# Kernel optimization log

Hardware: AMD Instinct MI355X
Metric: run time of the kernel (lower is better)

## Reference

```python
import jax, jax.numpy as jnp
import numpy as np

E = 16      # num_experts
H = 1024    # hidden_size
O = 1       # output_size
B = 4096    # batch
K = 2       # top-k (hard-coded in module)


def setup_inputs() -> dict:
    key = jax.random.key(0)
    ks = jax.random.split(key, 7)
    s_h = 1.0 / np.sqrt(H)
    inp = {
        "embeddings": jax.random.normal(ks[0], (B, H), dtype=jnp.float32),
        "router_w": jax.random.uniform(ks[1], (H, E), jnp.float32, -s_h, s_h),
        "router_b": jax.random.uniform(ks[2], (E,), jnp.float32, -s_h, s_h),
        "w1": jax.random.uniform(ks[3], (E, H, H), jnp.float32, -s_h, s_h),
        "b1": jax.random.uniform(ks[4], (E, H), jnp.float32, -s_h, s_h),
        "w2": jax.random.uniform(ks[5], (E, H, O), jnp.float32, -s_h, s_h),
        "b2": jax.random.uniform(ks[6], (E, O), jnp.float32, -s_h, s_h),
    }
    return inp


def reference(embeddings, router_w, router_b, w1, b1, w2, b2):
    # Router: top-2 experts per token, softmax over the 2 selected logits.
    logits = embeddings @ router_w + router_b                 # [B, E]
    top_vals, top_idx = jax.lax.top_k(logits, K)              # [B, K]
    top_w = jax.nn.softmax(top_vals, axis=-1)                 # [B, K]

    # Per-expert combine weight: w_e[b] = sum_k top_w[b,k] * (top_idx[b,k]==e)
    onehot = (top_idx[:, :, None] == jnp.arange(E)[None, None, :])  # [B, K, E]
    comb = jnp.einsum('bk,bke->eb', top_w, onehot.astype(top_w.dtype))  # [E, B]

    # Dense per-expert 2-layer MLP (small fixed E); masked-weighted combine
    # reproduces the gather/scatter-add exactly.
    h = jax.nn.relu(jnp.einsum('bh,ehd->ebd', embeddings, w1) + b1[:, None, :])  # [E, B, H]
    out = jnp.einsum('ebd,edo->ebo', h, w2) + b2[:, None, :]                      # [E, B, O]
    prediction = jnp.einsum('eb,ebo->bo', comb, out)                              # [B, O]
    return prediction
```

## Files before the change

kernel.cpp:

```cpp
#include <hip/hip_runtime.h>
#include <hip/hip_bf16.h>
#include <stdint.h>

#define E_EXP 16
#define H_DIM 1024
#define B_TOK 4096
#define BK 64
#define GBM 128
#define GBN 64
#define NSLOT 32
#define KS 16
#define KC 64
#define RTM 128
#define RSTRIDE (KC + 4)

typedef short bf16x8 __attribute__((ext_vector_type(8)));
typedef float f32x4 __attribute__((ext_vector_type(4)));

__device__ __forceinline__ unsigned short f2bf(float x) {
  union { float f; unsigned u; } v; v.f = x;
  unsigned r = v.u + 0x7FFFu + ((v.u >> 16) & 1u);
  return (unsigned short)(r >> 16);
}

__device__ __forceinline__ void gload_lds16(const void* g, void* l) {
  __builtin_amdgcn_global_load_lds(
      (const __attribute__((address_space(1))) void*)g,
      (__attribute__((address_space(3))) void*)l, 16, 0, 0);
}

__global__ __launch_bounds__(256) void k_prep(
    const float* __restrict__ emb, const float* __restrict__ rw,
    const float* __restrict__ w1, unsigned short* __restrict__ emb_bf,
    float* __restrict__ part, unsigned short* __restrict__ w1t)
{
  __shared__ __align__(16) char smem[RTM * RSTRIDE * 4 + KC * E_EXP * 4];
  const int tid = threadIdx.x;

  if (blockIdx.x < 512) {
    float* embL = (float*)smem;
    float* rwL  = (float*)(smem + RTM * RSTRIDE * 4);
    const int t0 = (blockIdx.x & 31) * RTM;
    const int ks = blockIdx.x >> 5;

#pragma unroll
    for (int it = 0; it < 8; ++it) {
      const int i = tid + 256 * it;
      const int row = i >> 4;
      const int c4 = i & 15;
      const size_t goff = (size_t)(t0 + row) * H_DIM + ks * KC + c4 * 4;
      const f32x4 v = *(const f32x4*)(emb + goff);
      ushort4 o;
      o.x = f2bf(v[0]); o.y = f2bf(v[1]); o.z = f2bf(v[2]); o.w = f2bf(v[3]);
      *(ushort4*)(emb_bf + goff) = o;
      *(f32x4*)(embL + row * RSTRIDE + c4 * 4) = v;
    }
    {
      const f32x4 v = *(const f32x4*)(rw + (size_t)ks * (KC * E_EXP) + tid * 4);
      *(f32x4*)(rwL + tid * 4) = v;
    }
    __syncthreads();

    const int w = tid >> 6, lane = tid & 63;
    const int tg = lane & 15, eg = lane >> 4;
    const int ta = w * 32 + tg, tb = ta + 16;

    f32x4 accA = {0.f, 0.f, 0.f, 0.f};
    f32x4 accB = {0.f, 0.f, 0.f, 0.f};
#pragma unroll
    for (int k4 = 0; k4 < KC / 4; ++k4) {
      const f32x4 e0 = *(const f32x4*)(embL + ta * RSTRIDE + k4 * 4);
      const f32x4 e1 = *(const f32x4*)(embL + tb * RSTRIDE + k4 * 4);
#pragma unroll
      for (int h = 0; h < 4; ++h) {
        const f32x4 r = *(const f32x4*)(rwL + (k4 * 4 + h) * E_EXP + eg * 4);
        accA += e0[h] * r;
        accB += e1[h] * r;
      }
    }
    *(f32x4*)(part + ((size_t)ks * B_TOK + t0 + ta) * E_EXP + eg * 4) = accA;
    *(f32x4*)(part + ((size_t)ks * B_TOK + t0 + tb) * E_EXP + eg * 4) = accB;
  } else {
    typedef unsigned short TileT[65];
    TileT* tile = (TileT*)smem;
    const int wb = blockIdx.x - 512;
    const int e  = wb >> 8;
    const int ht = (wb >> 4) & 15;
    const int dt = wb & 15;
    const float* src = w1 + ((size_t)e * H_DIM + ht * 64) * H_DIM + dt * 64;
    const int tr = tid >> 4;
    const int tc = tid & 15;
#pragma unroll
    for (int i = 0; i < 4; ++i) {
      const int r = tr + i * 16;
      const float4 v = *(const float4*)(src + (size_t)r * H_DIM + tc * 4);
      tile[r][tc * 4 + 0] = f2bf(v.x);
      tile[r][tc * 4 + 1] = f2bf(v.y);
      tile[r][tc * 4 + 2] = f2bf(v.z);
      tile[r][tc * 4 + 3] = f2bf(v.w);
    }
    __syncthreads();
    unsigned short* dst = w1t + ((size_t)e * H_DIM + dt * 64) * H_DIM + ht * 64;
    const int wr = tid >> 3;
    const int wc = tid & 7;
#pragma unroll
    for (int i = 0; i < 2; ++i) {
      const int r = wr + i * 32;
      ushort4 t0, t1;
      t0.x = tile[wc * 8 + 0][r]; t0.y = tile[wc * 8 + 1][r];
      t0.z = tile[wc * 8 + 2][r]; t0.w = tile[wc * 8 + 3][r];
      t1.x = tile[wc * 8 + 4][r]; t1.y = tile[wc * 8 + 5][r];
      t1.z = tile[wc * 8 + 6][r]; t1.w = tile[wc * 8 + 7][r];
      *(ushort4*)(dst + (size_t)r * H_DIM + wc * 8) = t0;
      *(ushort4*)(dst + (size_t)r * H_DIM + wc * 8 + 4) = t1;
    }
  }
}

__global__ __launch_bounds__(256) void k_router_select(
    const float* __restrict__ part, const float* __restrict__ rb,
    int* __restrict__ counts, int* __restrict__ lists,
    int4* __restrict__ meta, float2* __restrict__ wts)
{
  __shared__ int lcnt[E_EXP];
  __shared__ int base[E_EXP];
  const int tid = threadIdx.x;
  const int t = blockIdx.x * 256 + tid;
  if (tid < E_EXP) lcnt[tid] = 0;

  float lg[16];
#pragma unroll
  for (int q = 0; q < 4; ++q) {
    const f32x4 b = *(const f32x4*)(rb + q * 4);
    lg[q * 4 + 0] = b[0]; lg[q * 4 + 1] = b[1];
    lg[q * 4 + 2] = b[2]; lg[q * 4 + 3] = b[3];
  }
#pragma unroll
  for (int s = 0; s < KS; ++s) {
#pragma unroll
    for (int q = 0; q < 4; ++q) {
      const f32x4 v = *(const f32x4*)(part + ((size_t)s * B_TOK + t) * E_EXP + q * 4);
      lg[q * 4 + 0] += v[0]; lg[q * 4 + 1] += v[1];
      lg[q * 4 + 2] += v[2]; lg[q * 4 + 3] += v[3];
    }
  }

  float best = -1e30f; int b0 = 0;
#pragma unroll
  for (int e = 0; e < 16; ++e)
    if (lg[e] > best) { best = lg[e]; b0 = e; }
  float best2 = -1e30f; int b1i = 0;
#pragma unroll
  for (int e = 0; e < 16; ++e)
    if (e != b0 && lg[e] > best2) { best2 = lg[e]; b1i = e; }

  __syncthreads();
  const int l0 = atomicAdd(&lcnt[b0], 1);
  const int l1 = atomicAdd(&lcnt[b1i], 1);
  __syncthreads();
  if (tid < E_EXP) base[tid] = atomicAdd(&counts[tid], lcnt[tid]);
  __syncthreads();

  const int p0 = base[b0] + l0;
  const int p1 = base[b1i] + l1;
  lists[b0 * B_TOK + p0] = t;
  lists[b1i * B_TOK + p1] = t;
  meta[t] = make_int4(b0, b1i, p0, p1);
  const float e1v = expf(best2 - best);
  const float w0 = 1.f / (1.f + e1v);
  wts[t] = make_float2(w0, e1v * w0);
}

__global__ __launch_bounds__(256, 4) void k_moe_gemm(
    const unsigned short* __restrict__ emb_bf,
    const unsigned short* __restrict__ w1t,
    const float* __restrict__ b1, const float* __restrict__ w2,
    const int* __restrict__ counts, const int* __restrict__ lists,
    float* __restrict__ outbuf)
{
  const int bid = blockIdx.x;
  const int xcd = bid & 7;
  const int j = bid >> 3;
  const int e  = xcd + 8 * (j >> 7);
  const int r  = j & 127;
  const int nb = r >> 3;
  const int mbg = r & 7;
  const int cnt = counts[e];

  __shared__ unsigned short lA[GBM * BK];
  __shared__ unsigned short lB[GBN * BK];
  __shared__ int toks[GBM];

  const int tid = threadIdx.x;
  const int w = tid >> 6, lane = tid & 63;
  const int scb = ((lane & 7) * 16) ^ ((lane >> 3) << 4);
  const int wm = w >> 1, wn = w & 1;
  const int lr = lane & 15, lg = lane >> 4;

  const unsigned short* w1tb = w1t + ((size_t)e * H_DIM + nb * GBN) * H_DIM;
  const float* b1e = b1 + (size_t)e * H_DIM + nb * GBN;
  const float* w2e = w2 + (size_t)e * H_DIM + nb * GBN;

  const unsigned short* bSrc[2];
#pragma unroll
  for (int i = 0; i < 2; ++i) {
    const int n = (w * 2 + i) * 8 + (lane >> 3);
    bSrc[i] = w1tb + (size_t)n * H_DIM + (scb >> 1);
  }

  for (int mb = mbg; mb * GBM < cnt; mb += 8) {
    if (tid < GBM) {
      const int p = mb * GBM + tid;
      toks[tid] = lists[e * B_TOK + (p < cnt ? p : 0)];
    }
    __syncthreads();

    const unsigned short* aSrc[4];
#pragma unroll
    for (int i = 0; i < 4; ++i) {
      const int row = (w * 4 + i) * 8 + (lane >> 3);
      aSrc[i] = emb_bf + (size_t)toks[row] * H_DIM + (scb >> 1);
    }

    f32x4 acc[4][2];
#pragma unroll
    for (int m = 0; m < 4; ++m)
#pragma unroll
      for (int n = 0; n < 2; ++n) acc[m][n] = (f32x4){0.f, 0.f, 0.f, 0.f};

    for (int k0 = 0; k0 < H_DIM; k0 += BK) {
#pragma unroll
      for (int i = 0; i < 4; ++i)
        gload_lds16(aSrc[i] + k0, (char*)lA + (w * 4 + i) * 1024);
#pragma unroll
      for (int i = 0; i < 2; ++i)
        gload_lds16(bSrc[i] + k0, (char*)lB + (w * 2 + i) * 1024);
      __syncthreads();

#pragma unroll
      for (int kk = 0; kk < 2; ++kk) {
        const int kb = kk * 64 + lg * 16;
        bf16x8 af[4], bfr[2];
#pragma unroll
        for (int m = 0; m < 4; ++m) {
          const int row = wm * 64 + m * 16 + lr;
          af[m] = *(const bf16x8*)((const char*)lA + row * 128 + (kb ^ ((row & 7) << 4)));
        }
#pragma unroll
        for (int n = 0; n < 2; ++n) {
          const int row = wn * 32 + n * 16 + lr;
          bfr[n] = *(const bf16x8*)((const char*)lB + row * 128 + (kb ^ ((row & 7) << 4)));
        }
        __builtin_amdgcn_s_setprio(1);
#pragma unroll
        for (int m = 0; m < 4; ++m)
#pragma unroll
          for (int n = 0; n < 2; ++n)
            acc[m][n] = __builtin_amdgcn_mfma_f32_16x16x32_bf16(af[m], bfr[n], acc[m][n], 0, 0, 0);
        __builtin_amdgcn_s_setprio(0);
      }
      __syncthreads();
    }

    float rs[4][4];
#pragma unroll
    for (int m = 0; m < 4; ++m)
#pragma unroll
      for (int r4 = 0; r4 < 4; ++r4) rs[m][r4] = 0.f;

#pragma unroll
    for (int n = 0; n < 2; ++n) {
      const int d = wn * 32 + n * 16 + lr;
      const float bb = b1e[d];
      const float ww = w2e[d];
#pragma unroll
      for (int m = 0; m < 4; ++m)
#pragma unroll
        for (int r4 = 0; r4 < 4; ++r4) {
          float v = acc[m][n][r4] + bb;
          v = fmaxf(v, 0.f);
          rs[m][r4] = fmaf(v, ww, rs[m][r4]);
        }
    }
#pragma unroll
    for (int mask = 8; mask >= 1; mask >>= 1) {
#pragma unroll
      for (int m = 0; m < 4; ++m)
#pragma unroll
        for (int r4 = 0; r4 < 4; ++r4) rs[m][r4] += __shfl_xor(rs[m][r4], mask, 64);
    }

    if (lr == 0) {
      const int slot = nb * 2 + wn;
      float* ob = outbuf + ((size_t)slot * E_EXP + e) * B_TOK + mb * GBM;
#pragma unroll
      for (int m = 0; m < 4; ++m)
#pragma unroll
        for (int r4 = 0; r4 < 4; ++r4)
          ob[wm * 64 + m * 16 + lg * 4 + r4] = rs[m][r4];
    }
    __syncthreads();
  }
}

__global__ __launch_bounds__(256) void k_combine(
    const int4* __restrict__ meta, const float2* __restrict__ wts,
    const float* __restrict__ outbuf, const float* __restrict__ b2,
    float* __restrict__ out)
{
  const int t = blockIdx.x * 256 + threadIdx.x;
  if (t >= B_TOK) return;
  const int4 m = meta[t];
  const float2 w = wts[t];
  float o0 = b2[m.x], o1 = b2[m.y];
#pragma unroll
  for (int s = 0; s < NSLOT; ++s) {
    o0 += outbuf[((size_t)s * E_EXP + m.x) * B_TOK + m.z];
    o1 += outbuf[((size_t)s * E_EXP + m.y) * B_TOK + m.w];
  }
  out[t] = w.x * o0 + w.y * o1;
}

extern "C" void kernel_launch(void* const* d_in, const int* in_sizes, int n_in,
                              void* d_out, int out_size, void* d_ws, size_t ws_size,
                              hipStream_t stream)
{
  const float* emb = (const float*)d_in[0];
  const float* rw  = (const float*)d_in[1];
  const float* rb  = (const float*)d_in[2];
  const float* w1  = (const float*)d_in[3];
  const float* b1  = (const float*)d_in[4];
  const float* w2  = (const float*)d_in[5];
  const float* b2  = (const float*)d_in[6];
  float* out = (float*)d_out;

  char* ws = (char*)d_ws;
  size_t cur = 0;
  auto alloc = [&](size_t bytes) -> void* {
    void* p = ws + cur;
    cur += (bytes + 255) & ~(size_t)255;
    return p;
  };
  int*            counts = (int*)alloc(64);
  int4*           meta   = (int4*)alloc((size_t)B_TOK * 16);
  float2*         wts    = (float2*)alloc((size_t)B_TOK * 8);
  int*            lists  = (int*)alloc((size_t)E_EXP * B_TOK * 4);
  float*          outbuf = (float*)alloc((size_t)NSLOT * E_EXP * B_TOK * 4);
  float*          part   = (float*)alloc((size_t)KS * B_TOK * E_EXP * 4);
  unsigned short* emb_bf = (unsigned short*)alloc((size_t)B_TOK * H_DIM * 2);
  unsigned short* w1t    = (unsigned short*)alloc((size_t)E_EXP * H_DIM * H_DIM * 2);

  hipMemsetAsync(counts, 0, 64, stream);
  k_prep<<<dim3(512 + 4096), 256, 0, stream>>>(emb, rw, w1, emb_bf, part, w1t);
  k_router_select<<<B_TOK / 256, 256, 0, stream>>>(part, rb, counts, lists, meta, wts);
  k_moe_gemm<<<dim3(2048), 256, 0, stream>>>(emb_bf, w1t, b1, w2, counts, lists, outbuf);
  k_combine<<<B_TOK / 256, 256, 0, stream>>>(meta, wts, outbuf, b2, out);
}
```

Before: 85.64 us.

## Switch MoE GEMM to single-wave 64x64 tiles and fold counts reset into prep

The MoE GEMM goes from 256-thread blocks with 128x64 tiles to single-wavefront 64-thread blocks with 64x64 tiles, launching twice as many blocks. Because each block is one wave, the __syncthreads barriers become explicit waitcnt instructions, and token indices are read straight from the lists without staging them in LDS. The aim is to drop workgroup synchronisation and spread the variable per-expert token counts more finely across CUs. The trade-off is no overlap between loads and compute within a block and more total reads of the B tile. The counts memset is also moved into the prep kernel to save one launch.

Measured after the change: 76.96 us. -10.1%, faster.

```diff
diff --git a/kernel.cpp b/kernel.cpp
--- a/kernel.cpp
+++ b/kernel.cpp
@@ -6,9 +6,9 @@
 #define H_DIM 1024
 #define B_TOK 4096
 #define BK 64
-#define GBM 128
-#define GBN 64
-#define NSLOT 32
+#define WBM 64
+#define WBN 64
+#define NSLOT 16
 #define KS 16
 #define KC 64
 #define RTM 128
@@ -32,10 +32,13 @@
 __global__ __launch_bounds__(256) void k_prep(
     const float* __restrict__ emb, const float* __restrict__ rw,
     const float* __restrict__ w1, unsigned short* __restrict__ emb_bf,
-    float* __restrict__ part, unsigned short* __restrict__ w1t)
+    float* __restrict__ part, unsigned short* __restrict__ w1t,
+    int* __restrict__ counts)
 {
   __shared__ __align__(16) char smem[RTM * RSTRIDE * 4 + KC * E_EXP * 4];
   const int tid = threadIdx.x;
+
+  if (blockIdx.x == 0 && tid < E_EXP) counts[tid] = 0;
 
   if (blockIdx.x < 512) {
     float* embL = (float*)smem;
@@ -171,7 +174,7 @@
   wts[t] = make_float2(w0, e1v * w0);
 }
 
-__global__ __launch_bounds__(256, 4) void k_moe_gemm(
+__global__ __launch_bounds__(64) void k_moe_gemm(
     const unsigned short* __restrict__ emb_bf,
     const unsigned short* __restrict__ w1t,
     const float* __restrict__ b1, const float* __restrict__ w2,
@@ -181,85 +184,82 @@
   const int bid = blockIdx.x;
   const int xcd = bid & 7;
   const int j = bid >> 3;
-  const int e  = xcd + 8 * (j >> 7);
-  const int r  = j & 127;
-  const int nb = r >> 3;
-  const int mbg = r & 7;
+  const int e  = xcd + 8 * (j >> 8);
+  const int r  = j & 255;
+  const int nb = r >> 4;
+  const int mbg = r & 15;
   const int cnt = counts[e];
 
-  __shared__ unsigned short lA[GBM * BK];
-  __shared__ unsigned short lB[GBN * BK];
-  __shared__ int toks[GBM];
-
-  const int tid = threadIdx.x;
-  const int w = tid >> 6, lane = tid & 63;
+  __shared__ unsigned short lA[WBM * BK];
+  __shared__ unsigned short lB[WBN * BK];
+
+  const int lane = threadIdx.x;
   const int scb = ((lane & 7) * 16) ^ ((lane >> 3) << 4);
-  const int wm = w >> 1, wn = w & 1;
   const int lr = lane & 15, lg = lane >> 4;
 
-  const unsigned short* w1tb = w1t + ((size_t)e * H_DIM + nb * GBN) * H_DIM;
-  const float* b1e = b1 + (size_t)e * H_DIM + nb * GBN;
-  const float* w2e = w2 + (size_t)e * H_DIM + nb * GBN;
-
-  const unsigned short* bSrc[2];
-#pragma unroll
-  for (int i = 0; i < 2; ++i) {
-    const int n = (w * 2 + i) * 8 + (lane >> 3);
+  const unsigned short* w1tb = w1t + ((size_t)e * H_DIM + nb * WBN) * H_DIM;
+  const float* b1e = b1 + (size_t)e * H_DIM + nb * WBN;
+  const float* w2e = w2 + (size_t)e * H_DIM + nb * WBN;
+
+  const unsigned short* bSrc[8];
+#pragma unroll
+  for (int i = 0; i < 8; ++i) {
+    const int n = i * 8 + (lane >> 3);
     bSrc[i] = w1tb + (size_t)n * H_DIM + (scb >> 1);
   }
 
-  for (int mb = mbg; mb * GBM < cnt; mb += 8) {
-    if (tid < GBM) {
-      const int p = mb * GBM + tid;
-      toks[tid] = lists[e * B_TOK + (p < cnt ? p : 0)];
-    }
-    __syncthreads();
-
-    const unsigned short* aSrc[4];
-#pragma unroll
-    for (int i = 0; i < 4; ++i) {
-      const int row = (w * 4 + i) * 8 + (lane >> 3);
-      aSrc[i] = emb_bf + (size_t)toks[row] * H_DIM + (scb >> 1);
-    }
-
-    f32x4 acc[4][2];
+  for (int mb = mbg; mb * WBM < cnt; mb += 16) {
+    const int base = mb * WBM;
+
+    const unsigned short* aSrc[8];
+#pragma unroll
+    for (int i = 0; i < 8; ++i) {
+      const int p = base + i * 8 + (lane >> 3);
+      const int tok = lists[e * B_TOK + (p < cnt ? p : 0)];
+      aSrc[i] = emb_bf + (size_t)tok * H_DIM + (scb >> 1);
+    }
+
+    f32x4 acc[4][4];
 #pragma unroll
     for (int m = 0; m < 4; ++m)
 #pragma unroll
-      for (int n = 0; n < 2; ++n) acc[m][n] = (f32x4){0.f, 0.f, 0.f, 0.f};
-
+      for (int n = 0; n < 4; ++n) acc[m][n] = (f32x4){0.f, 0.f, 0.f, 0.f};
+
+#pragma unroll 1
     for (int k0 = 0; k0 < H_DIM; k0 += BK) {
-#pragma unroll
-      for (int i = 0; i < 4; ++i)
-        gload_lds16(aSrc[i] + k0, (char*)lA + (w * 4 + i) * 1024);
-#pragma unroll
-      for (int i = 0; i < 2; ++i)
-        gload_lds16(bSrc[i] + k0, (char*)lB + (w * 2 + i) * 1024);
-      __syncthreads();
+      asm volatile("s_waitcnt lgkmcnt(0)" ::: "memory");
+      __builtin_amdgcn_sched_barrier(0);
+#pragma unroll
+      for (int i = 0; i < 8; ++i)
+        gload_lds16(aSrc[i] + k0, (char*)lA + i * 1024);
+#pragma unroll
+      for (int i = 0; i < 8; ++i)
+        gload_lds16(bSrc[i] + k0, (char*)lB + i * 1024);
+      asm volatile("s_waitcnt vmcnt(0)" ::: "memory");
+      __builtin_amdgcn_sched_barrier(0);
 
 #pragma unroll
       for (int kk = 0; kk < 2; ++kk) {
         const int kb = kk * 64 + lg * 16;
-        bf16x8 af[4], bfr[2];
+        bf16x8 af[4], bfr[4];
 #pragma unroll
         for (int m = 0; m < 4; ++m) {
-          const int row = wm * 64 + m * 16 + lr;
+          const int row = m * 16 + lr;
           af[m] = *(const bf16x8*)((const char*)lA + row * 128 + (kb ^ ((row & 7) << 4)));
         }
 #pragma unroll
-        for (int n = 0; n < 2; ++n) {
-          const int row = wn * 32 + n * 16 + lr;
+        for (int n = 0; n < 4; ++n) {
+          const int row = n * 16 + lr;
           bfr[n] = *(const bf16x8*)((const char*)lB + row * 128 + (kb ^ ((row & 7) << 4)));
         }
         __builtin_amdgcn_s_setprio(1);
 #pragma unroll
         for (int m = 0; m < 4; ++m)
 #pragma unroll
-          for (int n = 0; n < 2; ++n)
+          for (int n = 0; n < 4; ++n)
             acc[m][n] = __builtin_amdgcn_mfma_f32_16x16x32_bf16(af[m], bfr[n], acc[m][n], 0, 0, 0);
         __builtin_amdgcn_s_setprio(0);
       }
-      __syncthreads();
     }
 
     float rs[4][4];
@@ -269,8 +269,8 @@
       for (int r4 = 0; r4 < 4; ++r4) rs[m][r4] = 0.f;
 
 #pragma unroll
-    for (int n = 0; n < 2; ++n) {
-      const int d = wn * 32 + n * 16 + lr;
+    for (int n = 0; n < 4; ++n) {
+      const int d = n * 16 + lr;
       const float bb = b1e[d];
       const float ww = w2e[d];
 #pragma unroll
@@ -291,15 +291,13 @@
     }
 
     if (lr == 0) {
-      const int slot = nb * 2 + wn;
-      float* ob = outbuf + ((size_t)slot * E_EXP + e) * B_TOK + mb * GBM;
+      float* ob = outbuf + ((size_t)nb * E_EXP + e) * B_TOK + base;
 #pragma unroll
       for (int m = 0; m < 4; ++m)
 #pragma unroll
         for (int r4 = 0; r4 < 4; ++r4)
-          ob[wm * 64 + m * 16 + lg * 4 + r4] = rs[m][r4];
-    }
-    __syncthreads();
+          ob[m * 16 + lg * 4 + r4] = rs[m][r4];
+    }
   }
 }
 
@@ -350,9 +348,8 @@
   unsigned short* emb_bf = (unsigned short*)alloc((size_t)B_TOK * H_DIM * 2);
   unsigned short* w1t    = (unsigned short*)alloc((size_t)E_EXP * H_DIM * H_DIM * 2);
 
-  hipMemsetAsync(counts, 0, 64, stream);
-  k_prep<<<dim3(512 + 4096), 256, 0, stream>>>(emb, rw, w1, emb_bf, part, w1t);
+  k_prep<<<dim3(512 + 4096), 256, 0, stream>>>(emb, rw, w1, emb_bf, part, w1t, counts);
   k_router_select<<<B_TOK / 256, 256, 0, stream>>>(part, rb, counts, lists, meta, wts);
-  k_moe_gemm<<<dim3(2048), 256, 0, stream>>>(emb_bf, w1t, b1, w2, counts, lists, outbuf);
+  k_moe_gemm<<<dim3(4096), 64, 0, stream>>>(emb_bf, w1t, b1, w2, counts, lists, outbuf);
   k_combine<<<B_TOK / 256, 256, 0, stream>>>(meta, wts, outbuf, b2, out);
 }
```
